# Performance work log

Hardware: AMD Instinct MI355X
Metric: run time of the kernel (lower is better)

Reference implementation:

```python
import jax, jax.numpy as jnp
import numpy as np

B, S, H, NH = 2, 2048, 512, 8
DK = H // NH


def setup_inputs() -> dict:
    key = jax.random.key(0)
    ks = jax.random.split(key, 12)
    inp = {
        "query": jax.random.normal(ks[0], (B, S, H), dtype=jnp.float32),
        "key": jax.random.normal(ks[1], (B, S, H), dtype=jnp.float32),
        "value": jax.random.normal(ks[2], (B, S, H), dtype=jnp.float32),
        "bias": jax.random.normal(ks[3], (B, 1, S, S), dtype=jnp.float32),
        "mask": jax.random.randint(ks[4], (B, S), 0, 2, dtype=jnp.int32),
        "Wq": jax.random.normal(ks[5], (H, H), dtype=jnp.float32) * 0.02,
        "bq": jax.random.normal(ks[6], (H,), dtype=jnp.float32) * 0.02,
        "Wk": jax.random.normal(ks[7], (H, H), dtype=jnp.float32) * 0.02,
        "bk": jax.random.normal(ks[8], (H,), dtype=jnp.float32) * 0.02,
        "Wv": jax.random.normal(ks[9], (H, H), dtype=jnp.float32) * 0.02,
        "bv": jax.random.normal(ks[10], (H,), dtype=jnp.float32) * 0.02,
    }
    return inp


def reference(query, key, value, bias, mask, Wq, bq, Wk, bk, Wv, bv):
    b = query.shape[0]
    # torch nn.Linear: x @ W.T + b, then split heads -> [B, h, S, d_k]
    def proj(x, W, bb):
        y = x @ W.T + bb
        return y.reshape(b, -1, NH, DK).transpose(0, 2, 1, 3)

    q = proj(query, Wq, bq)
    k = proj(key, Wk, bk)
    v = proj(value, Wv, bv)

    score = jnp.einsum("bhqd,bhkd->bhqk", q, k) / np.sqrt(DK).astype(np.float32)
    # NOTE: the source swaps bias/mask when calling attention():
    #   the 0/1 mask is ADDED to the scores...
    mask_add = mask.reshape(b, 1, 1, -1).astype(score.dtype)
    score = score + mask_add
    #   ...and the float bias is used for the masked_fill (bias == 0 -> -1e30).
    score = jnp.where(bias == 0, jnp.asarray(-1e30, score.dtype), score)
    attn = jax.nn.softmax(score, axis=-1)  # dropout=None in the source call
    x = jnp.einsum("bhqk,bhkd->bhqd", attn, v)
    return x.transpose(0, 2, 1, 3).reshape(b, -1, NH * DK)
```

## Files before the change

### kernel.cpp

```cpp
#include <hip/hip_runtime.h>
#include <hip/hip_bf16.h>
#include <stdint.h>

#define B_  2
#define S_  2048
#define H_  512
#define NH_ 8
#define DK_ 64

typedef __bf16 bf16x8 __attribute__((ext_vector_type(8)));
typedef short  s16x4  __attribute__((ext_vector_type(4)));
typedef float  f32x4  __attribute__((ext_vector_type(4)));

static __device__ __forceinline__ uint32_t pk2(float a, float b) {
  __hip_bfloat162 h = __float22bfloat162_rn(float2{a, b});
  uint32_t u;
  __builtin_memcpy(&u, &h, 4);
  return u;
}
static __device__ __forceinline__ uint4 pkf8(float4 a, float4 b) {
  return uint4{pk2(a.x, a.y), pk2(a.z, a.w), pk2(b.x, b.y), pk2(b.z, b.w)};
}

static __device__ __forceinline__ f32x4 mfma_k16(s16x4 a, s16x4 b, f32x4 c) {
#if defined(__HIP_DEVICE_COMPILE__)
  return __builtin_amdgcn_mfma_f32_16x16x16bf16_1k(a, b, c, 0, 0, 0);
#else
  (void)a; (void)b;
  return c;
#endif
}

typedef const __attribute__((address_space(1))) uint32_t* gas_t;
typedef __attribute__((address_space(3))) uint32_t* las_t;
static __device__ __forceinline__ void cp16(const void* g, void* l) {
  __builtin_amdgcn_global_load_lds((gas_t)g, (las_t)l, 16, 0, 0);
}

struct ProjArgs {
  const float* X[3];
  const float* W[3];
  const float* Bv[3];
  uint16_t*    O[3];
  const float* bias;
  const int*   mask;
  uint32_t*    zrow;
  float*       fmL;
};

__global__ __launch_bounds__(256) void prep_proj_kernel(ProjArgs pa) {
  __shared__ __align__(16) char psm[24640];
  int bid = blockIdx.x, t = threadIdx.x;

  if (bid >= 768) {
    if (bid < 4864) {
      int r = bid - 768;
      uint32_t* wbuf = (uint32_t*)psm;
      const uint4* src = (const uint4*)(pa.bias + (size_t)r * 2048 + t * 8);
      uint4 a = src[0], b2 = src[1];
      bool z = ((a.x << 1) == 0u) | ((a.y << 1) == 0u) |
               ((a.z << 1) == 0u) | ((a.w << 1) == 0u) |
               ((b2.x << 1) == 0u) | ((b2.y << 1) == 0u) |
               ((b2.z << 1) == 0u) | ((b2.w << 1) == 0u);
      uint64_t m = __ballot(z);
      if ((t & 63) == 0) {
        uint32_t bits = 0;
#pragma unroll
        for (int c = 0; c < 8; c++)
          bits |= (uint32_t)(((m >> (8 * c)) & 0xFFull) != 0ull) << c;
        wbuf[t >> 6] = bits;
      }
      __syncthreads();
      if (t == 0)
        pa.zrow[r] = wbuf[0] | (wbuf[1] << 8) | (wbuf[2] << 16) | (wbuf[3] << 24);
    } else {
      const float LOG2E = 1.44269504088896340736f;
#pragma unroll
      for (int i = 0; i < 16; i++) {
        int idx = i * 256 + t;
        pa.fmL[idx] = (float)pa.mask[idx] * LOG2E;
      }
    }
    return;
  }

  int mat = bid / 256;
  int rem = bid & 255;
  int mtile = rem >> 3, dtile = rem & 7;
  int m0 = mtile * 128, n0 = dtile * 64;
  const float* X  = pa.X[mat];
  const float* Wt = pa.W[mat];
  const float* Bv = pa.Bv[mat];
  uint16_t*    O  = pa.O[mat];

  uint16_t (*Xs)[64] = (uint16_t (*)[64])psm;
  uint16_t (*Ws)[64] = (uint16_t (*)[64])(psm + 16384);

  int w = t >> 6, l = t & 63, lo = l & 15, g = l >> 4;
  int srow = t >> 1, shalf = t & 1;
  int wrow = t >> 2, wq = t & 3;

  const float* Xrow = X + (size_t)(m0 + srow) * 512 + shalf * 32;
  const float* Wrow = Wt + (size_t)(n0 + wrow) * 512 + wq * 16;

  f32x4 acc[2][4];
#pragma unroll
  for (int st = 0; st < 2; st++)
#pragma unroll
    for (int dt = 0; dt < 4; dt++) acc[st][dt] = (f32x4){0.f, 0.f, 0.f, 0.f};

  float4 xa[8], wa2[4];
  {
    const float4* sx = (const float4*)Xrow;
    const float4* sw = (const float4*)Wrow;
#pragma unroll
    for (int i = 0; i < 8; i++) xa[i] = sx[i];
#pragma unroll
    for (int i = 0; i < 4; i++) wa2[i] = sw[i];
  }

  for (int kb = 0; kb < 8; kb++) {
#pragma unroll
    for (int j = 0; j < 4; j++) {
      int s = (shalf * 4 + j) ^ (srow & 7);
      *(uint4*)&Xs[srow][s * 8] = pkf8(xa[2 * j], xa[2 * j + 1]);
    }
#pragma unroll
    for (int j = 0; j < 2; j++) {
      int s = (wq * 2 + j) ^ (wrow & 7);
      *(uint4*)&Ws[wrow][s * 8] = pkf8(wa2[2 * j], wa2[2 * j + 1]);
    }
    __syncthreads();
    if (kb < 7) {
      const float4* sx = (const float4*)(Xrow + (kb + 1) * 64);
      const float4* sw = (const float4*)(Wrow + (kb + 1) * 64);
#pragma unroll
      for (int i = 0; i < 8; i++) xa[i] = sx[i];
#pragma unroll
      for (int i = 0; i < 4; i++) wa2[i] = sw[i];
    }
#pragma unroll
    for (int kk = 0; kk < 2; kk++) {
      int seg = (kk * 4 + g) ^ (lo & 7);
      bf16x8 xf[2], wf[4];
#pragma unroll
      for (int st = 0; st < 2; st++)
        xf[st] = *(const bf16x8*)&Xs[w * 32 + st * 16 + lo][seg * 8];
#pragma unroll
      for (int dt = 0; dt < 4; dt++)
        wf[dt] = *(const bf16x8*)&Ws[dt * 16 + lo][seg * 8];
      if (mat < 2) {
#pragma unroll
        for (int st = 0; st < 2; st++)
#pragma unroll
          for (int dt = 0; dt < 4; dt++)
            acc[st][dt] = __builtin_amdgcn_mfma_f32_16x16x32_bf16(wf[dt], xf[st], acc[st][dt], 0, 0, 0);
      } else {
#pragma unroll
        for (int st = 0; st < 2; st++)
#pragma unroll
          for (int dt = 0; dt < 4; dt++)
            acc[st][dt] = __builtin_amdgcn_mfma_f32_16x16x32_bf16(xf[st], wf[dt], acc[st][dt], 0, 0, 0);
      }
    }
    __syncthreads();
  }

  if (mat < 2) {
    float scale = (mat == 0) ? 0.125f : 1.0f;
    float4 bv4[4];
#pragma unroll
    for (int dt = 0; dt < 4; dt++)
      bv4[dt] = *(const float4*)(Bv + n0 + dt * 16 + g * 4);
#pragma unroll
    for (int st = 0; st < 2; st++) {
      int ss = m0 + w * 32 + st * 16 + lo;
      int bb = ss >> 11, sIn = ss & 2047;
      uint16_t* obase = O + ((size_t)(bb * NH_ + dtile) * S_ + sIn) * DK_;
#pragma unroll
      for (int dt = 0; dt < 4; dt++) {
        float v0 = (acc[st][dt][0] + bv4[dt].x) * scale;
        float v1 = (acc[st][dt][1] + bv4[dt].y) * scale;
        float v2 = (acc[st][dt][2] + bv4[dt].z) * scale;
        float v3 = (acc[st][dt][3] + bv4[dt].w) * scale;
        uint2 pk{pk2(v0, v1), pk2(v2, v3)};
        *(uint2*)(obase + dt * 16 + g * 4) = pk;
      }
    }
  } else {
    float bval[4];
#pragma unroll
    for (int dt = 0; dt < 4; dt++) bval[dt] = Bv[n0 + dt * 16 + lo];
#pragma unroll
    for (int st = 0; st < 2; st++) {
      int m = m0 + w * 32 + st * 16 + g * 4;
      int bb = m >> 11, sIn = m & 2047;
#pragma unroll
      for (int dt = 0; dt < 4; dt++) {
        int dd = dt * 16 + lo;
        float v0 = acc[st][dt][0] + bval[dt];
        float v1 = acc[st][dt][1] + bval[dt];
        float v2 = acc[st][dt][2] + bval[dt];
        float v3 = acc[st][dt][3] + bval[dt];
        uint2 pk{pk2(v0, v1), pk2(v2, v3)};
        *(uint2*)(O + ((size_t)(bb * NH_ + dtile) * DK_ + dd) * S_ + sIn) = pk;
      }
    }
  }
}

__global__ __launch_bounds__(256, 2) void attn_kernel(
    const uint16_t* __restrict__ Qb, const uint16_t* __restrict__ Kb,
    const uint16_t* __restrict__ Vt, const uint32_t* __restrict__ zrow,
    const float* __restrict__ fmL, const float* __restrict__ bias,
    float* __restrict__ out) {
  int bid = blockIdx.x;
  int bh = bid & 15, qtile = bid >> 4;
  int b = bh >> 3, h = bh & 7;
  int q0 = qtile * 32;
  int t = threadIdx.x;
  int w = t >> 6, l = t & 63, lo = l & 15, g = l >> 4;

  __shared__ __align__(16) char smem[32768];
  uint16_t* KsB = (uint16_t*)smem;
  uint16_t* VsB = (uint16_t*)(smem + 16384);

  const uint16_t* Qh = Qb + (size_t)bh * S_ * DK_;
  const uint16_t* Kh = Kb + (size_t)bh * S_ * DK_;
  const uint16_t* Vh = Vt + (size_t)bh * DK_ * S_;

  int lrow = l >> 3, lseg = (l & 7) ^ lrow;
  const uint16_t* kbase = Kh + (size_t)(w * 16 + lrow) * DK_ + lseg * 8;
  const uint16_t* vbase = Vh + (size_t)(w * 16 + lrow) * S_ + lseg * 8;
  uint16_t* kd0 = KsB + (w * 16) * 64;
  uint16_t* kd8 = KsB + (w * 16 + 8) * 64;
  uint16_t* vd0 = VsB + (w * 16) * 64;
  uint16_t* vd8 = VsB + (w * 16 + 8) * 64;

  uint32_t zall = zrow[(b << 11) + q0 + (l & 31)];
#pragma unroll
  for (int s = 1; s < 32; s <<= 1) zall |= __shfl_xor(zall, s);

  bf16x8 qf[2][2];
#pragma unroll
  for (int qt = 0; qt < 2; qt++)
#pragma unroll
    for (int kk = 0; kk < 2; kk++)
      qf[qt][kk] = *(const bf16x8*)(Qh + (size_t)(q0 + qt * 16 + lo) * DK_ + kk * 32 + g * 8);

  f32x4 o[4][2];
#pragma unroll
  for (int dt = 0; dt < 4; dt++)
#pragma unroll
    for (int qt = 0; qt < 2; qt++) o[dt][qt] = (f32x4){0.f, 0.f, 0.f, 0.f};
  float ts[2] = {0.f, 0.f};

  const float* fmrow = fmL + b * S_ + w * 16 + g * 4;
  const float LOG2E = 1.44269504088896340736f;

  cp16(kbase, kd0);
  cp16(kbase + 512, kd8);
  cp16(vbase, vd0);
  cp16(vbase + 8 * S_, vd8);

  for (int kb = 0; kb < 32; kb++) {
    int cur = kb & 1;
    int k0 = kb * 64;
    float4 mv4 = *(const float4*)(fmrow + k0);
    __syncthreads();
    if (kb + 1 < 32) {
      int kn = k0 + 64;
      int nb = (cur ^ 1) * 4096;
      cp16(kbase + (size_t)kn * 64, kd0 + nb);
      cp16(kbase + (size_t)kn * 64 + 512, kd8 + nb);
      cp16(vbase + kn, vd0 + nb);
      cp16(vbase + kn + 8 * S_, vd8 + nb);
    }
    const uint16_t* KsT = KsB + cur * 4096;
    const uint16_t* VsT = VsB + cur * 4096;

    s16x4 vf[4];
    {
      int s = (2 * w + (g >> 1)) ^ (lo & 7);
      int off = s * 8 + (g & 1) * 4;
#pragma unroll
      for (int dt = 0; dt < 4; dt++)
        vf[dt] = *(const s16x4*)(VsT + (dt * 16 + lo) * 64 + off);
    }
    bf16x8 kf[2];
#pragma unroll
    for (int kk = 0; kk < 2; kk++) {
      int s = (kk * 4 + g) ^ (lo & 7);
      kf[kk] = *(const bf16x8*)(KsT + (w * 16 + lo) * 64 + s * 8);
    }

    f32x4 c[2];
#pragma unroll
    for (int qt = 0; qt < 2; qt++) {
      f32x4 z = {0.f, 0.f, 0.f, 0.f};
      z = __builtin_amdgcn_mfma_f32_16x16x32_bf16(kf[0], qf[qt][0], z, 0, 0, 0);
      c[qt] = __builtin_amdgcn_mfma_f32_16x16x32_bf16(kf[1], qf[qt][1], z, 0, 0, 0);
    }

    float p[2][4];
    if (((zall >> kb) & 1u) == 0u) {
#pragma unroll
      for (int qt = 0; qt < 2; qt++) {
        p[qt][0] = __builtin_amdgcn_exp2f(__builtin_fmaf(c[qt][0], LOG2E, mv4.x));
        p[qt][1] = __builtin_amdgcn_exp2f(__builtin_fmaf(c[qt][1], LOG2E, mv4.y));
        p[qt][2] = __builtin_amdgcn_exp2f(__builtin_fmaf(c[qt][2], LOG2E, mv4.z));
        p[qt][3] = __builtin_amdgcn_exp2f(__builtin_fmaf(c[qt][3], LOG2E, mv4.w));
      }
    } else {
#pragma unroll
      for (int qt = 0; qt < 2; qt++) {
        float4 bz = *(const float4*)(bias + ((size_t)(b * S_ + q0 + qt * 16 + lo)) * S_ + k0 + w * 16 + g * 4);
        p[qt][0] = (bz.x == 0.f) ? 0.f : __builtin_amdgcn_exp2f(__builtin_fmaf(c[qt][0], LOG2E, mv4.x));
        p[qt][1] = (bz.y == 0.f) ? 0.f : __builtin_amdgcn_exp2f(__builtin_fmaf(c[qt][1], LOG2E, mv4.y));
        p[qt][2] = (bz.z == 0.f) ? 0.f : __builtin_amdgcn_exp2f(__builtin_fmaf(c[qt][2], LOG2E, mv4.z));
        p[qt][3] = (bz.w == 0.f) ? 0.f : __builtin_amdgcn_exp2f(__builtin_fmaf(c[qt][3], LOG2E, mv4.w));
      }
    }

    s16x4 pf[2];
#pragma unroll
    for (int qt = 0; qt < 2; qt++) {
      ts[qt] += (p[qt][0] + p[qt][1]) + (p[qt][2] + p[qt][3]);
      union { s16x4 v; uint32_t u[2]; } uu;
      uu.u[0] = pk2(p[qt][0], p[qt][1]);
      uu.u[1] = pk2(p[qt][2], p[qt][3]);
      pf[qt] = uu.v;
    }

#pragma unroll
    for (int dt = 0; dt < 4; dt++)
#pragma unroll
      for (int qt = 0; qt < 2; qt++)
        o[dt][qt] = mfma_k16(vf[dt], pf[qt], o[dt][qt]);
  }

  float* OT = (float*)smem;
  float* LS = (float*)(smem + 8448);
#pragma unroll
  for (int qt = 0; qt < 2; qt++) {
    float v = ts[qt];
    v += __shfl_xor(v, 16);
    v += __shfl_xor(v, 32);
    ts[qt] = v;
  }
  __syncthreads();
  if (g == 0) {
#pragma unroll
    for (int qt = 0; qt < 2; qt++) LS[(w * 2 + qt) * 16 + lo] = ts[qt];
  }
#pragma unroll
  for (int ww = 0; ww < 4; ww++) {
    if (w == ww) {
#pragma unroll
      for (int dt = 0; dt < 4; dt++)
#pragma unroll
        for (int qt = 0; qt < 2; qt++)
#pragma unroll
          for (int r = 0; r < 4; r++) {
            int idx = (dt * 16 + g * 4 + r) * 33 + qt * 16 + lo;
            if (ww == 0) OT[idx] = o[dt][qt][r];
            else         OT[idx] += o[dt][qt][r];
          }
    }
    __syncthreads();
  }
  {
    int q = t >> 3, dseg = (t & 7) * 8;
    int qt2 = q >> 4, lo2 = q & 15;
    float lsum = LS[(0 * 2 + qt2) * 16 + lo2] + LS[(1 * 2 + qt2) * 16 + lo2] +
                 LS[(2 * 2 + qt2) * 16 + lo2] + LS[(3 * 2 + qt2) * 16 + lo2];
    float linv = 1.0f / fmaxf(lsum, 1e-30f);
    float* ob = out + ((size_t)(b * S_ + q0 + q)) * H_ + h * DK_ + dseg;
#pragma unroll
    for (int i = 0; i < 2; i++) {
      float4 v;
      v.x = OT[(dseg + i * 4 + 0) * 33 + q] * linv;
      v.y = OT[(dseg + i * 4 + 1) * 33 + q] * linv;
      v.z = OT[(dseg + i * 4 + 2) * 33 + q] * linv;
      v.w = OT[(dseg + i * 4 + 3) * 33 + q] * linv;
      *(float4*)(ob + i * 4) = v;
    }
  }
}

extern "C" void kernel_launch(void* const* d_in, const int* in_sizes, int n_in,
                              void* d_out, int out_size, void* d_ws, size_t ws_size,
                              hipStream_t stream) {
  const float* query = (const float*)d_in[0];
  const float* key   = (const float*)d_in[1];
  const float* value = (const float*)d_in[2];
  const float* bias  = (const float*)d_in[3];
  const int*   mask  = (const int*)d_in[4];
  const float* Wq = (const float*)d_in[5];
  const float* bq = (const float*)d_in[6];
  const float* Wk = (const float*)d_in[7];
  const float* bk = (const float*)d_in[8];
  const float* Wv = (const float*)d_in[9];
  const float* bv = (const float*)d_in[10];

  char* ws = (char*)d_ws;
  uint32_t* zrow = (uint32_t*)ws;
  float*    fmL  = (float*)(ws + 16384);
  uint16_t* Qb = (uint16_t*)(ws + (size_t)(1 << 20));
  uint16_t* Kb = (uint16_t*)(ws + (size_t)(5 << 20));
  uint16_t* Vt = (uint16_t*)(ws + (size_t)(9 << 20));

  ProjArgs pa;
  pa.X[0] = query; pa.X[1] = key; pa.X[2] = value;
  pa.W[0] = Wq;    pa.W[1] = Wk;  pa.W[2] = Wv;
  pa.Bv[0] = bq;   pa.Bv[1] = bk; pa.Bv[2] = bv;
  pa.O[0] = Qb;    pa.O[1] = Kb;  pa.O[2] = Vt;
  pa.bias = bias;  pa.mask = mask;
  pa.zrow = zrow;  pa.fmL = fmL;

  prep_proj_kernel<<<4865, 256, 0, stream>>>(pa);

  attn_kernel<<<1024, 256, 0, stream>>>(Qb, Kb, Vt, zrow, fmL, bias, (float*)d_out);
}
```

Before: 173.4 us.

## Batch bias zero-scan to 8 rows per block and remap projection tiles per XCD

New measurement: 173.1 us. No clear change (-0.2%).

```diff
diff --git a/kernel.cpp b/kernel.cpp
--- a/kernel.cpp
+++ b/kernel.cpp
@@ -53,26 +53,36 @@
   int bid = blockIdx.x, t = threadIdx.x;
 
   if (bid >= 768) {
-    if (bid < 4864) {
-      int r = bid - 768;
-      uint32_t* wbuf = (uint32_t*)psm;
-      const uint4* src = (const uint4*)(pa.bias + (size_t)r * 2048 + t * 8);
-      uint4 a = src[0], b2 = src[1];
-      bool z = ((a.x << 1) == 0u) | ((a.y << 1) == 0u) |
-               ((a.z << 1) == 0u) | ((a.w << 1) == 0u) |
-               ((b2.x << 1) == 0u) | ((b2.y << 1) == 0u) |
-               ((b2.z << 1) == 0u) | ((b2.w << 1) == 0u);
-      uint64_t m = __ballot(z);
-      if ((t & 63) == 0) {
-        uint32_t bits = 0;
-#pragma unroll
-        for (int c = 0; c < 8; c++)
-          bits |= (uint32_t)(((m >> (8 * c)) & 0xFFull) != 0ull) << c;
-        wbuf[t >> 6] = bits;
+    if (bid < 1280) {
+      int rr = bid - 768;
+      const float* base = pa.bias + (size_t)rr * 8 * 2048 + t * 8;
+      uint4 a[8], b2[8];
+#pragma unroll
+      for (int i = 0; i < 8; i++) {
+        const uint4* src = (const uint4*)(base + (size_t)i * 2048);
+        a[i] = src[0]; b2[i] = src[1];
+      }
+      uint32_t (*wbuf)[4] = (uint32_t (*)[4])psm;
+      int wv = t >> 6, ln = t & 63;
+#pragma unroll
+      for (int i = 0; i < 8; i++) {
+        bool z = ((a[i].x << 1) == 0u) | ((a[i].y << 1) == 0u) |
+                 ((a[i].z << 1) == 0u) | ((a[i].w << 1) == 0u) |
+                 ((b2[i].x << 1) == 0u) | ((b2[i].y << 1) == 0u) |
+                 ((b2[i].z << 1) == 0u) | ((b2[i].w << 1) == 0u);
+        uint64_t m = __ballot(z);
+        if (ln == 0) {
+          uint32_t bits = 0;
+#pragma unroll
+          for (int c = 0; c < 8; c++)
+            bits |= (uint32_t)(((m >> (8 * c)) & 0xFFull) != 0ull) << c;
+          wbuf[i][wv] = bits;
+        }
       }
       __syncthreads();
-      if (t == 0)
-        pa.zrow[r] = wbuf[0] | (wbuf[1] << 8) | (wbuf[2] << 16) | (wbuf[3] << 24);
+      if (t < 8)
+        pa.zrow[rr * 8 + t] = wbuf[t][0] | (wbuf[t][1] << 8) |
+                              (wbuf[t][2] << 16) | (wbuf[t][3] << 24);
     } else {
       const float LOG2E = 1.44269504088896340736f;
 #pragma unroll
@@ -84,9 +94,10 @@
     return;
   }
 
-  int mat = bid / 256;
-  int rem = bid & 255;
-  int mtile = rem >> 3, dtile = rem & 7;
+  int xcd = bid & 7, j = bid >> 3;
+  int gi = ((j >> 3) << 3) | xcd;
+  int dtile = j & 7;
+  int mat = gi >> 5, mtile = gi & 31;
   int m0 = mtile * 128, n0 = dtile * 64;
   const float* X  = pa.X[mat];
   const float* Wt = pa.W[mat];
@@ -121,14 +132,14 @@
 
   for (int kb = 0; kb < 8; kb++) {
 #pragma unroll
-    for (int j = 0; j < 4; j++) {
-      int s = (shalf * 4 + j) ^ (srow & 7);
-      *(uint4*)&Xs[srow][s * 8] = pkf8(xa[2 * j], xa[2 * j + 1]);
-    }
-#pragma unroll
-    for (int j = 0; j < 2; j++) {
-      int s = (wq * 2 + j) ^ (wrow & 7);
-      *(uint4*)&Ws[wrow][s * 8] = pkf8(wa2[2 * j], wa2[2 * j + 1]);
+    for (int j2 = 0; j2 < 4; j2++) {
+      int s = (shalf * 4 + j2) ^ (srow & 7);
+      *(uint4*)&Xs[srow][s * 8] = pkf8(xa[2 * j2], xa[2 * j2 + 1]);
+    }
+#pragma unroll
+    for (int j2 = 0; j2 < 2; j2++) {
+      int s = (wq * 2 + j2) ^ (wrow & 7);
+      *(uint4*)&Ws[wrow][s * 8] = pkf8(wa2[2 * j2], wa2[2 * j2 + 1]);
     }
     __syncthreads();
     if (kb < 7) {
@@ -418,7 +429,7 @@
   pa.bias = bias;  pa.mask = mask;
   pa.zrow = zrow;  pa.fmL = fmL;
 
-  prep_proj_kernel<<<4865, 256, 0, stream>>>(pa);
+  prep_proj_kernel<<<1281, 256, 0, stream>>>(pa);
 
   attn_kernel<<<1024, 256, 0, stream>>>(Qb, Kb, Vt, zrow, fmL, bias, (float*)d_out);
 }
```
